# Performance work log

Hardware: AMD Instinct MI355X
Metric: run time of the kernel (lower is better)

## Reference

```python
import jax, jax.numpy as jnp
import numpy as np

D_MODEL = 256
N_HEADS = 8
N_LEVELS = 4
N_POINTS = 4
SHAPES = [(128, 128), (64, 64), (32, 32), (16, 16)]  # (H, W) per level


def _query_hw(Lq):
    h = int(Lq ** 0.5)
    w = Lq // h
    if h * w != Lq:
        facs = [(i, Lq // i) for i in range(1, int(Lq ** 0.5) + 1) if Lq % i == 0]
        h, w = min(facs, key=lambda t: abs(t[0] - t[1]))
    return h, w


def _grid_sample(img, grid):
    # img: [B, D, H, W]; grid: [B, Lq, P, 2] in [-1,1] (x, y)
    # bilinear, padding_mode='zeros', align_corners=False
    B, D, H, W = img.shape
    gx, gy = grid[..., 0], grid[..., 1]
    x = ((gx + 1.0) * W - 1.0) * 0.5
    y = ((gy + 1.0) * H - 1.0) * 0.5
    x0 = jnp.floor(x)
    y0 = jnp.floor(y)
    wx1 = x - x0
    wy1 = y - y0
    wx0 = 1.0 - wx1
    wy0 = 1.0 - wy1
    x0i = x0.astype(jnp.int32)
    y0i = y0.astype(jnp.int32)
    x1i = x0i + 1
    y1i = y0i + 1
    img_flat = img.reshape(B, D, H * W)

    def gather(yi, xi):
        valid = (xi >= 0) & (xi < W) & (yi >= 0) & (yi < H)
        idx = jnp.clip(yi, 0, H - 1) * W + jnp.clip(xi, 0, W - 1)  # [B,Lq,P]
        v = jnp.take_along_axis(img_flat, idx.reshape(B, 1, -1), axis=2)
        v = v.reshape(B, D, *yi.shape[1:])  # [B,D,Lq,P]
        return v * valid[:, None].astype(img.dtype)

    return (gather(y0i, x0i) * (wy0 * wx0)[:, None]
            + gather(y0i, x1i) * (wy0 * wx1)[:, None]
            + gather(y1i, x0i) * (wy1 * wx0)[:, None]
            + gather(y1i, x1i) * (wy1 * wx1)[:, None])


def _forward(query, input_flatten, spatial_shapes,
             W_off, b_off, W_attn, b_attn, W_val, b_val, W_out, b_out):
    N, Lq, C = query.shape
    M, L, P = N_HEADS, N_LEVELS, N_POINTS
    D = C // M
    shapes = np.asarray(spatial_shapes)  # static

    value = (input_flatten @ W_val + b_val).reshape(N, -1, M, D)
    off = (query @ W_off + b_off).reshape(N, Lq, M, L, P, 2)
    attn = jax.nn.softmax((query @ W_attn + b_attn).reshape(N, Lq, M, L * P), axis=-1)
    attn = attn.reshape(N, Lq, M, L, P)

    # normalized reference grid derived from Len_q (2D branch)
    qh, qw = _query_hw(Lq)
    ry, rx = jnp.meshgrid(jnp.linspace(0.5, qh - 0.5, qh) / qh,
                          jnp.linspace(0.5, qw - 0.5, qw) / qw, indexing='ij')
    ref = jnp.stack([rx.reshape(-1), ry.reshape(-1)], axis=-1)  # [Lq, 2] (x,y)
    norm = jnp.asarray(np.stack([shapes[:, 1], shapes[:, 0]], -1), jnp.float32)  # [L,2]=(W,H)
    loc = ref[None, :, None, None, None, :] + off / norm[None, None, None, :, None, :]
    grids = 2.0 * loc - 1.0  # [N,Lq,M,L,P,2]

    starts = np.concatenate([[0], np.cumsum(shapes[:, 0] * shapes[:, 1])])
    sampled = []
    for l in range(L):
        H, W = int(shapes[l, 0]), int(shapes[l, 1])
        v = value[:, starts[l]:starts[l + 1]]            # [N, H*W, M, D]
        v = v.transpose(0, 2, 3, 1).reshape(N * M, D, H, W)
        g = grids[:, :, :, l].transpose(0, 2, 1, 3, 4).reshape(N * M, Lq, P, 2)
        sampled.append(_grid_sample(v, g))               # [NM, D, Lq, P]

    vals = jnp.stack(sampled, axis=-2)                   # [NM, D, Lq, L, P]
    # faithful to original: values flattened (P, L)-major, weights (L, P)-major
    vals = vals.transpose(0, 1, 2, 4, 3).reshape(N * M, D, Lq, P * L)
    w = attn.transpose(0, 2, 1, 3, 4).reshape(N * M, 1, Lq, L * P)
    out = (vals * w).sum(-1).reshape(N, M * D, Lq).transpose(0, 2, 1)  # [N,Lq,C]
    return out @ W_out + b_out


def setup_inputs():
    key = jax.random.key(0)
    ks = jax.random.split(key, 12)
    N, Lq, C = 2, 16384, D_MODEL
    M, L, P = N_HEADS, N_LEVELS, N_POINTS
    Lin = sum(h * w for h, w in SHAPES)
    s = 0.02
    # sampling_offsets bias: original directional grid init
    thetas = np.arange(M, dtype=np.float32) * (2.0 * np.pi / M)
    gi = np.stack([np.cos(thetas), np.sin(thetas)], -1)
    gi = gi / np.abs(gi).max(-1, keepdims=True)
    gi = np.tile(gi.reshape(M, 1, 1, 2), (1, L, P, 1))
    for i in range(P):
        gi[:, :, i, :] *= (i + 1)
    inp = {
        'query': jax.random.normal(ks[0], (N, Lq, C), jnp.float32),
        'reference_points': jax.random.uniform(ks[1], (N, Lq, L, 2), jnp.float32),
        'input_flatten': jax.random.normal(ks[2], (N, Lin, C), jnp.float32),
        'spatial_shapes': jnp.array(SHAPES, jnp.int32),
        'level_start_index': jnp.array(np.concatenate([[0], np.cumsum([h * w for h, w in SHAPES[:-1]])]), jnp.int32),
        'W_off': jax.random.normal(ks[3], (C, M * L * P * 2), jnp.float32) * s,
        'b_off': jnp.asarray(gi.reshape(-1), jnp.float32),
        'W_attn': jax.random.normal(ks[4], (C, M * L * P), jnp.float32) * s,
        'b_attn': jnp.zeros((M * L * P,), jnp.float32),
        'W_val': jax.random.normal(ks[5], (C, C), jnp.float32) * (1.0 / np.sqrt(C)),
        'b_val': jnp.zeros((C,), jnp.float32),
        'W_out': jax.random.normal(ks[6], (C, C), jnp.float32) * (1.0 / np.sqrt(C)),
        'b_out': jnp.zeros((C,), jnp.float32),
    }
    return inp


def reference(query, reference_points, input_flatten, spatial_shapes, level_start_index,
              W_off, b_off, W_attn, b_attn, W_val, b_val, W_out, b_out):
    assert reference_points.shape[-1] == 2
    return _forward(query, input_flatten, spatial_shapes,
                    W_off, b_off, W_attn, b_attn, W_val, b_val, W_out, b_out)
```

## Files before the change

kernel.cpp:

```cpp
#include <hip/hip_runtime.h>
#include <math.h>

#define NB   2
#define LQ   16384
#define CDIM 256
#define MH   8
#define DH   32
#define LIN  21760
#define NPIX (NB * LIN)

typedef __attribute__((ext_vector_type(8))) _Float16 f16x8;
typedef __attribute__((ext_vector_type(4))) _Float16 f16x4;
typedef __attribute__((ext_vector_type(4))) float    f32x4;

__device__ __forceinline__ void async16(const void* g, void* l) {
    __builtin_amdgcn_global_load_lds(
        (const __attribute__((address_space(1))) void*)g,
        (__attribute__((address_space(3))) void*)l,
        16, 0, 0);
}

__global__ __launch_bounds__(256) void tsplit_all_kernel(
    const float* __restrict__ Wv, const float* __restrict__ Wo,
    const float* __restrict__ Wf, const float* __restrict__ Wa,
    _Float16* __restrict__ Wvt, _Float16* __restrict__ Wot, _Float16* __restrict__ Wct)
{
    const int i = blockIdx.x * 256 + threadIdx.x;
    const int r = i >> 8;
    const int kk = i & 255;
    if (r < 256) {
        Wvt[r * 256 + kk] = (_Float16)Wv[kk * 256 + r];
    } else if (r < 512) {
        const int n = r - 256;
        Wot[n * 256 + kk] = (_Float16)Wo[kk * 256 + n];
    } else if (r < 768) {
        const int n = r - 512;
        Wct[n * 256 + kk] = (_Float16)Wf[kk * 256 + n];
    } else {
        const int n = r - 768;
        Wct[(256 + n) * 256 + kk] = (_Float16)Wa[kk * 128 + n];
    }
}

template <int OUT_MODE, bool A_F32>
__global__ __launch_bounds__(256) void gemm_f16(
    const void* __restrict__ Araw, const _Float16* __restrict__ Bt,
    const float* __restrict__ bias0, const float* __restrict__ bias1,
    void* __restrict__ C0, void* __restrict__ C1,
    int M, int N, int K, int N0)
{
    __shared__ __align__(16) char AshRaw[A_F32 ? 128 * 32 * 4 : 128 * 32 * 2];
    __shared__ _Float16 Bsh[128 * 32];

    const int tid  = threadIdx.x;
    const int wave = tid >> 6, lane = tid & 63;
    const int quad = lane >> 4, l16 = lane & 15;
    const int bm = blockIdx.y * 128;
    const int bn = blockIdx.x * 128;
    const int wrow = wave * 32;

    f32x4 acc[2][8] = {};

    const int s0 = tid,        row0 = s0 >> 2, kg0 = (s0 & 3) << 3;
    const int s1 = tid + 256,  row1 = s1 >> 2, kg1 = (s1 & 3) << 3;

    for (int k0 = 0; k0 < K; k0 += 32) {
        if (A_F32) {
            const float* A = (const float*)Araw;
            float* AshF = (float*)AshRaw;
            #pragma unroll
            for (int j = 0; j < 4; ++j) {
                const int s = tid + 256 * j;
                async16(A + (size_t)(bm + (s >> 3)) * K + k0 + ((s & 7) << 2),
                        AshF + s * 4);
            }
        } else {
            const _Float16* A = (const _Float16*)Araw;
            _Float16* Ash = (_Float16*)AshRaw;
            async16(A + (size_t)(bm + row0) * K + k0 + kg0, Ash + s0 * 8);
            async16(A + (size_t)(bm + row1) * K + k0 + kg1, Ash + s1 * 8);
        }
        async16(Bt + (size_t)(bn + row0) * K + k0 + kg0, Bsh + s0 * 8);
        async16(Bt + (size_t)(bn + row1) * K + k0 + kg1, Bsh + s1 * 8);
        __syncthreads();

        f16x8 ah[2];
        #pragma unroll
        for (int r = 0; r < 2; ++r) {
            if (A_F32) {
                const float* AshF = (const float*)AshRaw;
                const float* ap = &AshF[(wrow + r * 16 + l16) * 32 + quad * 8];
                const f32x4 a0 = *(const f32x4*)ap;
                const f32x4 a1 = *(const f32x4*)(ap + 4);
                f16x8 h;
                h[0] = (_Float16)a0[0]; h[1] = (_Float16)a0[1];
                h[2] = (_Float16)a0[2]; h[3] = (_Float16)a0[3];
                h[4] = (_Float16)a1[0]; h[5] = (_Float16)a1[1];
                h[6] = (_Float16)a1[2]; h[7] = (_Float16)a1[3];
                ah[r] = h;
            } else {
                const _Float16* Ash = (const _Float16*)AshRaw;
                ah[r] = *(const f16x8*)&Ash[(wrow + r * 16 + l16) * 32 + quad * 8];
            }
        }
        #pragma unroll
        for (int half = 0; half < 2; ++half) {
            f16x8 bh[4];
            #pragma unroll
            for (int c = 0; c < 4; ++c)
                bh[c] = *(const f16x8*)&Bsh[(half * 64 + c * 16 + l16) * 32 + quad * 8];
            #pragma unroll
            for (int r = 0; r < 2; ++r)
                #pragma unroll
                for (int c = 0; c < 4; ++c)
                    acc[r][half * 4 + c] = __builtin_amdgcn_mfma_f32_16x16x32_f16(
                        ah[r], bh[c], acc[r][half * 4 + c], 0, 0, 0);
        }
        __syncthreads();
    }

    void* Cb; const float* bb; int ldc, coff;
    if (bn < N0) { Cb = C0; bb = bias0; ldc = N0;     coff = 0;  }
    else         { Cb = C1; bb = bias1; ldc = N - N0; coff = N0; }
    #pragma unroll
    for (int c = 0; c < 8; ++c) {
        const int col = bn + c * 16 + l16 - coff;
        const float bia = bb[col];
        #pragma unroll
        for (int r = 0; r < 2; ++r)
            #pragma unroll
            for (int i = 0; i < 4; ++i) {
                const int rr = bm + wrow + r * 16 + quad * 4 + i;
                const float v = acc[r][c][i] + bia;
                if (OUT_MODE == 2)
                    ((_Float16*)Cb)[((size_t)(col >> 5) * NPIX + rr) * 32 + (col & 31)] = (_Float16)v;
                else if (OUT_MODE == 1)
                    ((_Float16*)Cb)[(size_t)rr * ldc + col] = (_Float16)v;
                else
                    ((float*)Cb)[(size_t)rr * ldc + col] = v;
            }
    }
}

__global__ __launch_bounds__(256) void sample_kernel_v8(
    const _Float16* __restrict__ value,
    const float* __restrict__ off,
    const float* __restrict__ attn,
    _Float16* __restrict__ outv)
{
    __shared__ __align__(16) float lds_task[8][516];

    const int tid = threadIdx.x;
    const int qbase = blockIdx.x * 4;

    #pragma unroll
    for (int j = 0; j < 2; ++j) {
        const int t  = tid + 256 * j;
        const int q  = t >> 7;
        const int m  = (t >> 4) & 7;
        const int pt = t & 15;
        const int l  = pt >> 2;
        const int p  = pt & 3;
        const int qi = qbase + q;
        const int lq = qi & (LQ - 1);
        const int n  = qi >> 14;

        const int Hl = 128 >> l;
        const int STARTS[4] = {0, 16384, 20480, 21504};

        const float2 oxy = *(const float2*)&off[(size_t)qi * 256 + m * 32 + pt * 2];

        const float logit = attn[(size_t)qi * 128 + m * 16 + p * 4 + l];
        float mx = logit;
        #pragma unroll
        for (int d = 1; d < 16; d <<= 1) mx = fmaxf(mx, __shfl_xor(mx, d, 16));
        const float e = __expf(logit - mx);
        float sm = e;
        #pragma unroll
        for (int d = 1; d < 16; d <<= 1) sm += __shfl_xor(sm, d, 16);
        const float w = e / sm;

        const float refx = ((lq & 127) + 0.5f) * (1.0f / 128.0f);
        const float refy = ((lq >> 7)  + 0.5f) * (1.0f / 128.0f);

        const float x = refx * (float)Hl + oxy.x - 0.5f;
        const float y = refy * (float)Hl + oxy.y - 0.5f;
        const float x0f = floorf(x), y0f = floorf(y);
        const int x0 = (int)x0f, y0 = (int)y0f;
        const int x1 = x0 + 1,  y1 = y0 + 1;
        const float fx = x - x0f, fy = y - y0f;
        const float gx = 1.f - fx, gy = 1.f - fy;

        const float vx0 = (x0 >= 0 && x0 < Hl) ? 1.f : 0.f;
        const float vx1 = (x1 >= 0 && x1 < Hl) ? 1.f : 0.f;
        const float vy0 = (y0 >= 0 && y0 < Hl) ? 1.f : 0.f;
        const float vy1 = (y1 >= 0 && y1 < Hl) ? 1.f : 0.f;

        const int x0c = min(max(x0, 0), Hl - 1);
        const int x1c = min(max(x1, 0), Hl - 1);
        const int y0c = min(max(y0, 0), Hl - 1);
        const int y1c = min(max(y1, 0), Hl - 1);

        const int base = m * (NPIX * 32) + (n * LIN + STARTS[l]) * 32;
        const int i00 = base + (y0c * Hl + x0c) * 32;
        const int i01 = base + (y0c * Hl + x1c) * 32;
        const int i10 = base + (y1c * Hl + x0c) * 32;
        const int i11 = base + (y1c * Hl + x1c) * 32;

        float4 wv;
        wv.x = w * gy * gx * vy0 * vx0;
        wv.y = w * gy * fx * vy0 * vx1;
        wv.z = w * fy * gx * vy1 * vx0;
        wv.w = w * fy * fx * vy1 * vx1;

        float* dst = &lds_task[m][(q * 16 + pt) * 8];
        *(float4*)dst = wv;
        int4 iv = {i00, i01, i10, i11};
        *(int4*)(dst + 4) = iv;
    }
    __syncthreads();

    const int q  = tid >> 6;
    const int m  = (tid >> 3) & 7;
    const int d4 = tid & 7;
    const int qi = qbase + q;

    const _Float16* vbase = value + d4 * 4;

    float4 acc = {0.f, 0.f, 0.f, 0.f};
    #pragma unroll
    for (int pt = 0; pt < 16; ++pt) {
        const float* td = &lds_task[m][(q * 16 + pt) * 8];
        const float4 wv = *(const float4*)td;
        const int4  iv = *(const int4*)(td + 4);
        const f16x4 v00 = *(const f16x4*)&vbase[iv.x];
        const f16x4 v01 = *(const f16x4*)&vbase[iv.y];
        const f16x4 v10 = *(const f16x4*)&vbase[iv.z];
        const f16x4 v11 = *(const f16x4*)&vbase[iv.w];
        acc.x += wv.x * (float)v00[0] + wv.y * (float)v01[0] + wv.z * (float)v10[0] + wv.w * (float)v11[0];
        acc.y += wv.x * (float)v00[1] + wv.y * (float)v01[1] + wv.z * (float)v10[1] + wv.w * (float)v11[1];
        acc.z += wv.x * (float)v00[2] + wv.y * (float)v01[2] + wv.z * (float)v10[2] + wv.w * (float)v11[2];
        acc.w += wv.x * (float)v00[3] + wv.y * (float)v01[3] + wv.z * (float)v10[3] + wv.w * (float)v11[3];
    }

    f16x4 o;
    o.x = (_Float16)acc.x; o.y = (_Float16)acc.y;
    o.z = (_Float16)acc.z; o.w = (_Float16)acc.w;
    *(f16x4*)&outv[(size_t)qi * 256 + m * 32 + d4 * 4] = o;
}

extern "C" void kernel_launch(void* const* d_in, const int* in_sizes, int n_in,
                              void* d_out, int out_size, void* d_ws, size_t ws_size,
                              hipStream_t stream)
{
    const float* query         = (const float*)d_in[0];
    const float* input_flatten = (const float*)d_in[2];
    const float* W_off  = (const float*)d_in[5];
    const float* b_off  = (const float*)d_in[6];
    const float* W_attn = (const float*)d_in[7];
    const float* b_attn = (const float*)d_in[8];
    const float* W_val  = (const float*)d_in[9];
    const float* b_val  = (const float*)d_in[10];
    const float* W_out  = (const float*)d_in[11];
    const float* b_out  = (const float*)d_in[12];
    float* out = (float*)d_out;

    char* w = (char*)d_ws;
    _Float16* Sf16 = (_Float16*)w;
    _Float16* value16 = (_Float16*)(w + 23068672);
    float*    attnbuf = (float*)(w + 67633152);
    _Float16* Wvt = (_Float16*)(w + 84410368);
    _Float16* Wot = Wvt + 65536;
    _Float16* Wct = Wot + 65536;
    float* offbuf = out;

    dim3 blk(256);

    tsplit_all_kernel<<<896, blk, 0, stream>>>(W_val, W_out, W_off, W_attn, Wvt, Wot, Wct);

    gemm_f16<2, true><<<dim3(2, 340), blk, 0, stream>>>(
        input_flatten, Wvt, b_val, b_val, value16, value16, 43520, 256, 256, 256);

    gemm_f16<0, true><<<dim3(3, 256), blk, 0, stream>>>(
        query, Wct, b_off, b_attn, offbuf, attnbuf, 32768, 384, 256, 256);

    sample_kernel_v8<<<8192, blk, 0, stream>>>(value16, offbuf, attnbuf, Sf16);

    gemm_f16<0, false><<<dim3(2, 256), blk, 0, stream>>>(
        Sf16, Wot, b_out, b_out, out, out, 32768, 256, 256, 256);
}
```

Baseline: 254.0 us.

## Double-buffer GEMM LDS tiles with XOR swizzle and vectorize epilogue stores

The GEMM now stages the next K tile into a second LDS buffer while computing on the current one. It XOR-swizzles the A and B tile layouts to avoid LDS bank conflicts, swaps the MFMA operands so each lane holds four consecutive output columns, and writes results with float4 or f16x4 vector stores. The sampling kernel now uses precomputed byte offsets with unsigned addressing and a vectorized accumulate. These changes target load latency, bank conflicts and scalar store overhead, at the cost of doubling GEMM LDS use, which may lower occupancy.

```diff
diff --git a/kernel.cpp b/kernel.cpp
--- a/kernel.cpp
+++ b/kernel.cpp
@@ -49,8 +49,8 @@
     void* __restrict__ C0, void* __restrict__ C1,
     int M, int N, int K, int N0)
 {
-    __shared__ __align__(16) char AshRaw[A_F32 ? 128 * 32 * 4 : 128 * 32 * 2];
-    __shared__ _Float16 Bsh[128 * 32];
+    __shared__ __align__(16) char AshRaw[2][A_F32 ? 128 * 32 * 4 : 128 * 32 * 2];
+    __shared__ __align__(16) _Float16 Bsh[2][128 * 32];
 
     const int tid  = threadIdx.x;
     const int wave = tid >> 6, lane = tid & 63;
@@ -61,37 +61,51 @@
 
     f32x4 acc[2][8] = {};
 
-    const int s0 = tid,        row0 = s0 >> 2, kg0 = (s0 & 3) << 3;
-    const int s1 = tid + 256,  row1 = s1 >> 2, kg1 = (s1 & 3) << 3;
-
-    for (int k0 = 0; k0 < K; k0 += 32) {
+    const int sB0 = tid, sB1 = tid + 256;
+    const int rB0 = sB0 >> 2, rB1 = sB1 >> 2;
+    const int kB0 = ((sB0 & 3) ^ ((rB0 >> 1) & 3)) << 3;
+    const int kB1 = ((sB1 & 3) ^ ((rB1 >> 1) & 3)) << 3;
+
+    const int T = K >> 5;
+    int cur = 0;
+
+    auto stage = [&](int buf, int k0) {
         if (A_F32) {
             const float* A = (const float*)Araw;
-            float* AshF = (float*)AshRaw;
+            float* AshF = (float*)AshRaw[buf];
             #pragma unroll
             for (int j = 0; j < 4; ++j) {
                 const int s = tid + 256 * j;
-                async16(A + (size_t)(bm + (s >> 3)) * K + k0 + ((s & 7) << 2),
-                        AshF + s * 4);
+                const int row = s >> 3;
+                const int kg = ((s & 7) ^ (row & 7)) << 2;
+                async16(A + (size_t)(bm + row) * K + k0 + kg, AshF + s * 4);
             }
         } else {
             const _Float16* A = (const _Float16*)Araw;
-            _Float16* Ash = (_Float16*)AshRaw;
-            async16(A + (size_t)(bm + row0) * K + k0 + kg0, Ash + s0 * 8);
-            async16(A + (size_t)(bm + row1) * K + k0 + kg1, Ash + s1 * 8);
+            _Float16* Ash = (_Float16*)AshRaw[buf];
+            async16(A + (size_t)(bm + rB0) * K + k0 + kB0, Ash + sB0 * 8);
+            async16(A + (size_t)(bm + rB1) * K + k0 + kB1, Ash + sB1 * 8);
         }
-        async16(Bt + (size_t)(bn + row0) * K + k0 + kg0, Bsh + s0 * 8);
-        async16(Bt + (size_t)(bn + row1) * K + k0 + kg1, Bsh + s1 * 8);
-        __syncthreads();
+        async16(Bt + (size_t)(bn + rB0) * K + k0 + kB0, Bsh[buf] + sB0 * 8);
+        async16(Bt + (size_t)(bn + rB1) * K + k0 + kB1, Bsh[buf] + sB1 * 8);
+    };
+
+    stage(0, 0);
+    __syncthreads();
+
+    for (int t = 0; t < T; ++t) {
+        if (t + 1 < T) stage(cur ^ 1, (t + 1) << 5);
 
         f16x8 ah[2];
         #pragma unroll
         for (int r = 0; r < 2; ++r) {
+            const int arow = wrow + r * 16 + l16;
             if (A_F32) {
-                const float* AshF = (const float*)AshRaw;
-                const float* ap = &AshF[(wrow + r * 16 + l16) * 32 + quad * 8];
-                const f32x4 a0 = *(const f32x4*)ap;
-                const f32x4 a1 = *(const f32x4*)(ap + 4);
+                const float* AshF = (const float*)AshRaw[cur];
+                const int c0 = (2 * quad)     ^ (arow & 7);
+                const int c1 = (2 * quad + 1) ^ (arow & 7);
+                const f32x4 a0 = *(const f32x4*)&AshF[arow * 32 + c0 * 4];
+                const f32x4 a1 = *(const f32x4*)&AshF[arow * 32 + c1 * 4];
                 f16x8 h;
                 h[0] = (_Float16)a0[0]; h[1] = (_Float16)a0[1];
                 h[2] = (_Float16)a0[2]; h[3] = (_Float16)a0[3];
@@ -99,50 +113,62 @@
                 h[6] = (_Float16)a1[2]; h[7] = (_Float16)a1[3];
                 ah[r] = h;
             } else {
-                const _Float16* Ash = (const _Float16*)AshRaw;
-                ah[r] = *(const f16x8*)&Ash[(wrow + r * 16 + l16) * 32 + quad * 8];
+                const _Float16* Ash = (const _Float16*)AshRaw[cur];
+                ah[r] = *(const f16x8*)&Ash[arow * 32 + ((quad ^ ((arow >> 1) & 3)) << 3)];
             }
         }
         #pragma unroll
         for (int half = 0; half < 2; ++half) {
             f16x8 bh[4];
             #pragma unroll
-            for (int c = 0; c < 4; ++c)
-                bh[c] = *(const f16x8*)&Bsh[(half * 64 + c * 16 + l16) * 32 + quad * 8];
+            for (int c = 0; c < 4; ++c) {
+                const int brow = half * 64 + c * 16 + l16;
+                bh[c] = *(const f16x8*)&Bsh[cur][brow * 32 + ((quad ^ ((brow >> 1) & 3)) << 3)];
+            }
             #pragma unroll
             for (int r = 0; r < 2; ++r)
                 #pragma unroll
                 for (int c = 0; c < 4; ++c)
                     acc[r][half * 4 + c] = __builtin_amdgcn_mfma_f32_16x16x32_f16(
-                        ah[r], bh[c], acc[r][half * 4 + c], 0, 0, 0);
+                        bh[c], ah[r], acc[r][half * 4 + c], 0, 0, 0);
         }
         __syncthreads();
+        cur ^= 1;
     }
 
     void* Cb; const float* bb; int ldc, coff;
     if (bn < N0) { Cb = C0; bb = bias0; ldc = N0;     coff = 0;  }
     else         { Cb = C1; bb = bias1; ldc = N - N0; coff = N0; }
     #pragma unroll
-    for (int c = 0; c < 8; ++c) {
-        const int col = bn + c * 16 + l16 - coff;
-        const float bia = bb[col];
-        #pragma unroll
-        for (int r = 0; r < 2; ++r)
-            #pragma unroll
-            for (int i = 0; i < 4; ++i) {
-                const int rr = bm + wrow + r * 16 + quad * 4 + i;
-                const float v = acc[r][c][i] + bia;
-                if (OUT_MODE == 2)
-                    ((_Float16*)Cb)[((size_t)(col >> 5) * NPIX + rr) * 32 + (col & 31)] = (_Float16)v;
-                else if (OUT_MODE == 1)
-                    ((_Float16*)Cb)[(size_t)rr * ldc + col] = (_Float16)v;
-                else
-                    ((float*)Cb)[(size_t)rr * ldc + col] = v;
+    for (int cidx = 0; cidx < 8; ++cidx) {
+        const int col = bn + cidx * 16 + quad * 4 - coff;
+        const float4 bia = *(const float4*)&bb[col];
+        #pragma unroll
+        for (int r = 0; r < 2; ++r) {
+            const int rr = bm + wrow + r * 16 + l16;
+            float4 v;
+            v.x = acc[r][cidx][0] + bia.x;
+            v.y = acc[r][cidx][1] + bia.y;
+            v.z = acc[r][cidx][2] + bia.z;
+            v.w = acc[r][cidx][3] + bia.w;
+            if (OUT_MODE == 0) {
+                *(float4*)&((float*)Cb)[(size_t)rr * ldc + col] = v;
+            } else if (OUT_MODE == 1) {
+                f16x4 h;
+                h[0] = (_Float16)v.x; h[1] = (_Float16)v.y;
+                h[2] = (_Float16)v.z; h[3] = (_Float16)v.w;
+                *(f16x4*)&((_Float16*)Cb)[(size_t)rr * ldc + col] = h;
+            } else {
+                f16x4 h;
+                h[0] = (_Float16)v.x; h[1] = (_Float16)v.y;
+                h[2] = (_Float16)v.z; h[3] = (_Float16)v.w;
+                *(f16x4*)&((_Float16*)Cb)[((size_t)(col >> 5) * NPIX + rr) * 32 + (col & 31)] = h;
             }
-    }
-}
-
-__global__ __launch_bounds__(256) void sample_kernel_v8(
+        }
+    }
+}
+
+__global__ __launch_bounds__(256) void sample_kernel_v9(
     const _Float16* __restrict__ value,
     const float* __restrict__ off,
     const float* __restrict__ attn,
@@ -201,11 +227,11 @@
         const int y0c = min(max(y0, 0), Hl - 1);
         const int y1c = min(max(y1, 0), Hl - 1);
 
-        const int base = m * (NPIX * 32) + (n * LIN + STARTS[l]) * 32;
-        const int i00 = base + (y0c * Hl + x0c) * 32;
-        const int i01 = base + (y0c * Hl + x1c) * 32;
-        const int i10 = base + (y1c * Hl + x0c) * 32;
-        const int i11 = base + (y1c * Hl + x1c) * 32;
+        const int baseb = m * (NPIX * 64) + (n * LIN + STARTS[l]) * 64;
+        const int i00 = baseb + (y0c * Hl + x0c) * 64;
+        const int i01 = baseb + (y0c * Hl + x1c) * 64;
+        const int i10 = baseb + (y1c * Hl + x0c) * 64;
+        const int i11 = baseb + (y1c * Hl + x1c) * 64;
 
         float4 wv;
         wv.x = w * gy * gx * vy0 * vx0;
@@ -214,9 +240,9 @@
         wv.w = w * fy * fx * vy1 * vx1;
 
         float* dst = &lds_task[m][(q * 16 + pt) * 8];
-        *(float4*)dst = wv;
         int4 iv = {i00, i01, i10, i11};
-        *(int4*)(dst + 4) = iv;
+        *(int4*)dst = iv;
+        *(float4*)(dst + 4) = wv;
     }
     __syncthreads();
 
@@ -224,28 +250,29 @@
     const int m  = (tid >> 3) & 7;
     const int d4 = tid & 7;
     const int qi = qbase + q;
-
-    const _Float16* vbase = value + d4 * 4;
-
-    float4 acc = {0.f, 0.f, 0.f, 0.f};
+    const unsigned dd = (unsigned)(d4 * 8);
+    const char* vp = (const char*)value;
+
+    f32x4 acc = {0.f, 0.f, 0.f, 0.f};
     #pragma unroll
     for (int pt = 0; pt < 16; ++pt) {
         const float* td = &lds_task[m][(q * 16 + pt) * 8];
-        const float4 wv = *(const float4*)td;
-        const int4  iv = *(const int4*)(td + 4);
-        const f16x4 v00 = *(const f16x4*)&vbase[iv.x];
-        const f16x4 v01 = *(const f16x4*)&vbase[iv.y];
-        const f16x4 v10 = *(const f16x4*)&vbase[iv.z];
-        const f16x4 v11 = *(const f16x4*)&vbase[iv.w];
-        acc.x += wv.x * (float)v00[0] + wv.y * (float)v01[0] + wv.z * (float)v10[0] + wv.w * (float)v11[0];
-        acc.y += wv.x * (float)v00[1] + wv.y * (float)v01[1] + wv.z * (float)v10[1] + wv.w * (float)v11[1];
-        acc.z += wv.x * (float)v00[2] + wv.y * (float)v01[2] + wv.z * (float)v10[2] + wv.w * (float)v11[2];
-        acc.w += wv.x * (float)v00[3] + wv.y * (float)v01[3] + wv.z * (float)v10[3] + wv.w * (float)v11[3];
+        const int4  iv = *(const int4*)td;
+        const float4 wv = *(const float4*)(td + 4);
+        const f16x4 v00 = *(const f16x4*)(vp + ((unsigned)iv.x + dd));
+        const f16x4 v01 = *(const f16x4*)(vp + ((unsigned)iv.y + dd));
+        const f16x4 v10 = *(const f16x4*)(vp + ((unsigned)iv.z + dd));
+        const f16x4 v11 = *(const f16x4*)(vp + ((unsigned)iv.w + dd));
+        f32x4 f00 = {(float)v00[0], (float)v00[1], (float)v00[2], (float)v00[3]};
+        f32x4 f01 = {(float)v01[0], (float)v01[1], (float)v01[2], (float)v01[3]};
+        f32x4 f10 = {(float)v10[0], (float)v10[1], (float)v10[2], (float)v10[3]};
+        f32x4 f11 = {(float)v11[0], (float)v11[1], (float)v11[2], (float)v11[3]};
+        acc += wv.x * f00 + wv.y * f01 + wv.z * f10 + wv.w * f11;
     }
 
     f16x4 o;
-    o.x = (_Float16)acc.x; o.y = (_Float16)acc.y;
-    o.z = (_Float16)acc.z; o.w = (_Float16)acc.w;
+    o[0] = (_Float16)acc[0]; o[1] = (_Float16)acc[1];
+    o[2] = (_Float16)acc[2]; o[3] = (_Float16)acc[3];
     *(f16x4*)&outv[(size_t)qi * 256 + m * 32 + d4 * 4] = o;
 }
 
@@ -284,7 +311,7 @@
     gemm_f16<0, true><<<dim3(3, 256), blk, 0, stream>>>(
         query, Wct, b_off, b_attn, offbuf, attnbuf, 32768, 384, 256, 256);
 
-    sample_kernel_v8<<<8192, blk, 0, stream>>>(value16, offbuf, attnbuf, Sf16);
+    sample_kernel_v9<<<8192, blk, 0, stream>>>(value16, offbuf, attnbuf, Sf16);
 
     gemm_f16<0, false><<<dim3(2, 256), blk, 0, stream>>>(
         Sf16, Wot, b_out, b_out, out, out, 32768, 256, 256, 256);
```

Measured after the change: 258.4 us. About the same (+1.7%).
